# Kernel tuning notes

Measured on AMD Instinct MI355X. Metric: run time of the kernel, lower is better.

The kernel has to match this reference:

```python
import jax, jax.numpy as jnp
import numpy as np

D_MODEL = 2048
N_HEADS = 16
D_HEAD = D_MODEL // N_HEADS


def setup_inputs() -> dict:
    key = jax.random.key(0)
    ks = jax.random.split(key, 9)
    s = 1.0 / np.sqrt(D_MODEL)
    x = jax.random.normal(ks[0], (2, 2048, D_MODEL), dtype=jnp.float32)
    wq = jax.random.uniform(ks[1], (D_MODEL, D_MODEL), jnp.float32, -s, s)
    wk = jax.random.uniform(ks[2], (D_MODEL, D_MODEL), jnp.float32, -s, s)
    wv = jax.random.uniform(ks[3], (D_MODEL, D_MODEL), jnp.float32, -s, s)
    wo = jax.random.uniform(ks[4], (D_MODEL, D_MODEL), jnp.float32, -s, s)
    bq = jax.random.uniform(ks[5], (D_MODEL,), jnp.float32, -s, s)
    bk = jax.random.uniform(ks[6], (D_MODEL,), jnp.float32, -s, s)
    bv = jax.random.uniform(ks[7], (D_MODEL,), jnp.float32, -s, s)
    bo = jax.random.uniform(ks[8], (D_MODEL,), jnp.float32, -s, s)
    return {"x": x, "wq": wq, "bq": bq, "wk": wk, "bk": bk,
            "wv": wv, "bv": bv, "wo": wo, "bo": bo}


def reference(x, wq, bq, wk, bk, wv, bv, wo, bo):
    b, s, _ = x.shape
    # torch Linear: y = x @ W.T + b
    q = (jnp.einsum('bsd,ed->bse', x, wq) + bq).reshape(b, s, N_HEADS, D_HEAD)
    k = (jnp.einsum('bsd,ed->bse', x, wk) + bk).reshape(b, s, N_HEADS, D_HEAD)
    v = (jnp.einsum('bsd,ed->bse', x, wv) + bv).reshape(b, s, N_HEADS, D_HEAD)
    scale = 1.0 / np.sqrt(D_HEAD).astype(np.float32)
    # [b, h, s, s] attention scores (naive full materialization, as in source)
    attn = jnp.einsum('bqhd,bkhd->bhqk', q, k) * scale
    attn = jax.nn.softmax(attn, axis=-1)
    out = jnp.einsum('bhqk,bkhd->bqhd', attn, v).reshape(b, s, D_MODEL)
    return jnp.einsum('bsd,ed->bse', out, wo) + bo
```

## Files before the change

### kernel.cpp

```cpp
#include <hip/hip_runtime.h>

#define D_MODEL 2048
#define SEQ     2048
#define NB      2
#define NH      16
#define DH      128
#define MROWS   (NB*SEQ)
#define GK      2048
#define NT      (GK/64)

typedef __bf16 bf16x8 __attribute__((ext_vector_type(8)));
typedef float  f32x4  __attribute__((ext_vector_type(4)));
typedef unsigned short ushort8 __attribute__((ext_vector_type(8)));
typedef unsigned int   u32x4   __attribute__((ext_vector_type(4)));

__device__ __forceinline__ unsigned short f2bf(float f) {
  unsigned int u = __float_as_uint(f);
  u += 0x7FFFu + ((u >> 16) & 1u);
  return (unsigned short)(u >> 16);
}

__device__ __forceinline__ unsigned int cvtpk_bf16(float lo, float hi) {
  unsigned int r;
  asm("v_cvt_pk_bf16_f32 %0, %1, %2" : "=v"(r) : "v"(lo), "v"(hi));
  return r;
}

__device__ __forceinline__ void gload16(void* lds, const void* g) {
  __builtin_amdgcn_global_load_lds(
      (__attribute__((address_space(1))) void*)(g),
      (__attribute__((address_space(3))) void*)(lds), 16, 0, 0);
}

__global__ __launch_bounds__(256) void cast_all(
    const float* __restrict__ x,
    const float* __restrict__ w0, const float* __restrict__ w1,
    const float* __restrict__ w2, const float* __restrict__ w3,
    unsigned short* __restrict__ xb, unsigned short* __restrict__ wb) {
  int gb = blockIdx.x;
  const float* src;
  unsigned short* dst;
  int i;
  if (gb < 4096) {
    src = x; dst = xb; i = gb * 256 + threadIdx.x;
  } else {
    int g2 = gb - 4096;
    int which = g2 >> 11;
    src = (which == 0) ? w0 : (which == 1) ? w1 : (which == 2) ? w2 : w3;
    dst = wb + (size_t)which * 4194304;
    i = (g2 & 2047) * 256 + threadIdx.x;
  }
  const float4* p = (const float4*)src;
  float4 a = p[2*i], b = p[2*i+1];
  ushort8 o;
  o[0]=f2bf(a.x); o[1]=f2bf(a.y); o[2]=f2bf(a.z); o[3]=f2bf(a.w);
  o[4]=f2bf(b.x); o[5]=f2bf(b.y); o[6]=f2bf(b.z); o[7]=f2bf(b.w);
  ((ushort8*)dst)[i] = o;
}

__global__ __launch_bounds__(512, 2) void gemm192(
    const unsigned short* __restrict__ A,
    const unsigned short* __restrict__ B,
    const float* __restrict__ b0, const float* __restrict__ b1,
    const float* __restrict__ b2,
    unsigned short* __restrict__ qo, unsigned short* __restrict__ ko,
    unsigned short* __restrict__ vo)
{
  __shared__ char lds[2*57344];

  const int tid  = threadIdx.x;
  const int lane = tid & 63, wid = tid >> 6;
  const int la   = lane & 15, hi = lane >> 4;
  const int wm   = wid >> 2,  wn = wid & 3;

  const int xcd = (int)blockIdx.x & 7, ii = (int)blockIdx.x >> 3;
  const int bm  = ii >> 2;
  const int bn  = xcd * 4 + (ii & 3);

  const unsigned short* Ab = A + (size_t)(bm*256) * GK;
  const unsigned short* Bb = B + (size_t)(bn*192) * GK;

  f32x4 acc[8][3];
  #pragma unroll
  for (int m = 0; m < 8; m++)
    #pragma unroll
    for (int n = 0; n < 3; n++) acc[m][n] = f32x4{0.f,0.f,0.f,0.f};

#define STG_A1J(base_, kt, J) do {                                            \
    int idx = (J)*512 + tid;                                                  \
    int row = idx >> 3;                                                       \
    int c   = (idx & 7) << 4;                                                 \
    gload16((base_) + idx*16,                                                 \
            Ab + (size_t)row*GK + (kt)*64 + ((c ^ ((row&7)<<4)) >> 1));       \
  } while (0)

#define STG_BJ(base_, kt, J0, J1) do {                                        \
    _Pragma("unroll")                                                         \
    for (int j = (J0); j < (J1); j++) {                                       \
      int idx = j*512 + tid;                                                  \
      int row = idx >> 3;                                                     \
      int c   = (idx & 7) << 4;                                               \
      gload16((base_) + 32768 + idx*16,                                       \
              Bb + (size_t)row*GK + (kt)*64 + ((c ^ ((row&7)<<4)) >> 1));     \
    }                                                                         \
  } while (0)

  STG_BJ(lds, 0, 0, 3);
  STG_A1J(lds, 0, 0); STG_A1J(lds, 0, 2);
  STG_A1J(lds, 0, 1); STG_A1J(lds, 0, 3);
  asm volatile("s_waitcnt vmcnt(2)" ::: "memory");
  __builtin_amdgcn_s_barrier();

  const int xr = (la & 7) << 4;

  #pragma unroll 1
  for (int t = 0; t < NT; ++t) {
    const char* sa  = lds + (t&1)*57344;
    const char* sbp = sa + 32768;
    char* nb = lds + ((t+1)&1)*57344;
    const bool pf = (t + 1 < NT);

    bf16x8 bfr[3], aq[4];

    #pragma unroll
    for (int n = 0; n < 3; n++)
      bfr[n] = *(const bf16x8*)(sbp + (((wn*48 + n*16 + la)*128 + hi*16) ^ xr));
    #pragma unroll
    for (int m = 0; m < 4; m++)
      aq[m] = *(const bf16x8*)(sa + (((wm*128 + m*16 + la)*128 + hi*16) ^ xr));
    if (pf) STG_BJ(nb, t+1, 0, 3);
    asm volatile("s_waitcnt lgkmcnt(0)" ::: "memory");
    __builtin_amdgcn_sched_barrier(0);
    __builtin_amdgcn_s_setprio(1);
    #pragma unroll
    for (int m = 0; m < 4; m++)
      #pragma unroll
      for (int n = 0; n < 3; n++)
        acc[m][n] = __builtin_amdgcn_mfma_f32_16x16x32_bf16(aq[m], bfr[n], acc[m][n], 0, 0, 0);
    __builtin_amdgcn_s_setprio(0);
    if (pf) asm volatile("s_waitcnt vmcnt(3)" ::: "memory");
    else    asm volatile("s_waitcnt vmcnt(0)" ::: "memory");
    __builtin_amdgcn_s_barrier();

    #pragma unroll
    for (int m = 0; m < 4; m++)
      aq[m] = *(const bf16x8*)(sa + (((wm*128 + (m+4)*16 + la)*128 + hi*16) ^ xr));
    if (pf) { STG_A1J(nb, t+1, 0); STG_A1J(nb, t+1, 2); }
    asm volatile("s_waitcnt lgkmcnt(0)" ::: "memory");
    __builtin_amdgcn_sched_barrier(0);
    __builtin_amdgcn_s_setprio(1);
    #pragma unroll
    for (int m = 0; m < 4; m++)
      #pragma unroll
      for (int n = 0; n < 3; n++)
        acc[m+4][n] = __builtin_amdgcn_mfma_f32_16x16x32_bf16(aq[m], bfr[n], acc[m+4][n], 0, 0, 0);
    __builtin_amdgcn_s_setprio(0);
    __builtin_amdgcn_s_barrier();

    #pragma unroll
    for (int n = 0; n < 3; n++)
      bfr[n] = *(const bf16x8*)(sbp + (((wn*48 + n*16 + la)*128 + 64 + hi*16) ^ xr));
    #pragma unroll
    for (int m = 0; m < 4; m++)
      aq[m] = *(const bf16x8*)(sa + (((wm*128 + m*16 + la)*128 + 64 + hi*16) ^ xr));
    if (pf) { STG_A1J(nb, t+1, 1); STG_A1J(nb, t+1, 3); }
    asm volatile("s_waitcnt lgkmcnt(0)" ::: "memory");
    __builtin_amdgcn_sched_barrier(0);
    __builtin_amdgcn_s_setprio(1);
    #pragma unroll
    for (int m = 0; m < 4; m++)
      #pragma unroll
      for (int n = 0; n < 3; n++)
        acc[m][n] = __builtin_amdgcn_mfma_f32_16x16x32_bf16(aq[m], bfr[n], acc[m][n], 0, 0, 0);
    __builtin_amdgcn_s_setprio(0);
    __builtin_amdgcn_s_barrier();

    #pragma unroll
    for (int m = 0; m < 4; m++)
      aq[m] = *(const bf16x8*)(sa + (((wm*128 + (m+4)*16 + la)*128 + 64 + hi*16) ^ xr));
    asm volatile("s_waitcnt lgkmcnt(0)" ::: "memory");
    __builtin_amdgcn_sched_barrier(0);
    __builtin_amdgcn_s_setprio(1);
    #pragma unroll
    for (int m = 0; m < 4; m++)
      #pragma unroll
      for (int n = 0; n < 3; n++)
        acc[m+4][n] = __builtin_amdgcn_mfma_f32_16x16x32_bf16(aq[m], bfr[n], acc[m+4][n], 0, 0, 0);
    __builtin_amdgcn_s_setprio(0);
    if (pf) asm volatile("s_waitcnt vmcnt(2)" ::: "memory");
    else    asm volatile("s_waitcnt vmcnt(0)" ::: "memory");
    __builtin_amdgcn_s_barrier();
  }
#undef STG_A1J
#undef STG_BJ

  const int row0 = bm*256 + wm*128;
  const int col0 = bn*192 + wn*48;
  #pragma unroll
  for (int n = 0; n < 3; n++) {
    int col = col0 + n*16 + la;
    int mat = col >> 11;
    int c   = col & 2047;
    int h   = c >> 7, d = c & 127;
    const float* bp = (mat == 0) ? b0 : (mat == 1) ? b1 : b2;
    float bv = bp[c];
    #pragma unroll
    for (int m = 0; m < 8; m++)
      #pragma unroll
      for (int r = 0; r < 4; r++) {
        int row = row0 + m*16 + hi*4 + r;
        int bb  = row >> 11, s = row & (SEQ-1);
        unsigned short val = f2bf(acc[m][n][r] + bv);
        if (mat == 0) {
          qo[((size_t)(bb*NH + h)*SEQ + s)*DH + d] = val;
        } else if (mat == 1) {
          size_t base = ((size_t)(bb*NH + h)*SEQ + (size_t)(s >> 6)*64)*DH;
          int boff = (((s & 63) << 8) + (d << 1)) ^ ((s & 7) << 4);
          ko[base + (boff >> 1)] = val;
        } else {
          size_t base = ((size_t)(bb*NH + h)*SEQ + (size_t)(s >> 6)*64)*DH;
          int boff = ((d << 7) + ((s & 63) << 1)) ^ ((d & 7) << 4);
          vo[base + (boff >> 1)] = val;
        }
      }
  }
}

__global__ __launch_bounds__(512, 2) void gemm256(
    const unsigned short* __restrict__ A,
    const unsigned short* __restrict__ B,
    const float* __restrict__ b0,
    float* __restrict__ fo,
    int nbnx)
{
  __shared__ char lds[3*49152];

  const int tid  = threadIdx.x;
  const int lane = tid & 63, wid = tid >> 6;
  const int la   = lane & 15, hi = lane >> 4;
  const int wm   = wid >> 2,  wn = wid & 3;

  const int xcd = (int)blockIdx.x & 7, ii = (int)blockIdx.x >> 3;
  const int bm  = ii / nbnx;
  const int bn  = xcd * nbnx + ii % nbnx;

  const unsigned short* Ab = A + (size_t)(bm*128) * GK;
  const unsigned short* Bb = B + (size_t)(bn*256) * GK;

  f32x4 acc[4][4];
  #pragma unroll
  for (int m = 0; m < 4; m++)
    #pragma unroll
    for (int n = 0; n < 4; n++) acc[m][n] = f32x4{0.f,0.f,0.f,0.f};

#define STAGE_A(slot, kt) do {                                                \
    int sb_ = (slot) * 49152;                                                 \
    _Pragma("unroll")                                                         \
    for (int j = 0; j < 2; j++) {                                             \
      int idx = j*512 + tid;                                                  \
      int row = idx >> 3;                                                     \
      int c   = (idx & 7) << 4;                                               \
      gload16(lds + sb_ + idx*16,                                             \
              Ab + (size_t)row*GK + (kt)*64 + ((c ^ ((row&7)<<4)) >> 1));     \
    }                                                                         \
  } while (0)

#define STAGE_B(slot, kt) do {                                                \
    int sb_ = (slot) * 49152;                                                 \
    _Pragma("unroll")                                                         \
    for (int j = 0; j < 4; j++) {                                             \
      int idx = j*512 + tid;                                                  \
      int row = idx >> 3;                                                     \
      int c   = (idx & 7) << 4;                                               \
      gload16(lds + sb_ + 16384 + idx*16,                                     \
              Bb + (size_t)row*GK + (kt)*64 + ((c ^ ((row&7)<<4)) >> 1));     \
    }                                                                         \
  } while (0)

  STAGE_A(0, 0); STAGE_B(0, 0);
  STAGE_A(1, 1); STAGE_B(1, 1);

  int cs = 0, ps = 2;
  const int xr = (la & 7) << 4;

  #pragma unroll 1
  for (int t = 0; t < NT; ++t) {
    if (t + 1 < NT) asm volatile("s_waitcnt vmcnt(6)" ::: "memory");
    else            asm volatile("s_waitcnt vmcnt(0)" ::: "memory");
    __builtin_amdgcn_s_barrier();

    const char* sa  = lds + cs*49152;
    const char* sbp = sa + 16384;

    bf16x8 bfr[4][2], aA[2][2];
    #pragma unroll
    for (int n = 0; n < 4; n++)
      #pragma unroll
      for (int ks = 0; ks < 2; ks++)
        bfr[n][ks] = *(const bf16x8*)(sbp + (((wn*64 + n*16 + la)*128 + ks*64 + hi*16) ^ xr));
    #pragma unroll
    for (int m = 0; m < 2; m++)
      #pragma unroll
      for (int ks = 0; ks < 2; ks++)
        aA[m][ks] = *(const bf16x8*)(sa + (((wm*64 + m*16 + la)*128 + ks*64 + hi*16) ^ xr));

    if (t + 2 < NT) STAGE_A(ps, t + 2);

    asm volatile("s_waitcnt lgkmcnt(0)" ::: "memory");
    __builtin_amdgcn_sched_barrier(0);
    __builtin_amdgcn_s_setprio(1);
    #pragma unroll
    for (int m = 0; m < 2; m++)
      #pragma unroll
      for (int n = 0; n < 4; n++)
        #pragma unroll
        for (int ks = 0; ks < 2; ks++)
          acc[m][n] = __builtin_amdgcn_mfma_f32_16x16x32_bf16(aA[m][ks], bfr[n][ks], acc[m][n], 0, 0, 0);
    __builtin_amdgcn_s_setprio(0);
    __builtin_amdgcn_s_barrier();

    bf16x8 aB[2][2];
    #pragma unroll
    for (int m = 0; m < 2; m++)
      #pragma unroll
      for (int ks = 0; ks < 2; ks++)
        aB[m][ks] = *(const bf16x8*)(sa + (((wm*64 + (m+2)*16 + la)*128 + ks*64 + hi*16) ^ xr));

    if (t + 2 < NT) STAGE_B(ps, t + 2);

    asm volatile("s_waitcnt lgkmcnt(0)" ::: "memory");
    __builtin_amdgcn_sched_barrier(0);
    __builtin_amdgcn_s_setprio(1);
    #pragma unroll
    for (int m = 0; m < 2; m++)
      #pragma unroll
      for (int n = 0; n < 4; n++)
        #pragma unroll
        for (int ks = 0; ks < 2; ks++)
          acc[m+2][n] = __builtin_amdgcn_mfma_f32_16x16x32_bf16(aB[m][ks], bfr[n][ks], acc[m+2][n], 0, 0, 0);
    __builtin_amdgcn_s_setprio(0);

    cs = cs + 1; if (cs == 3) cs = 0;
    ps = ps + 1; if (ps == 3) ps = 0;
  }
#undef STAGE_A
#undef STAGE_B

  const int row0 = bm*128 + wm*64;
  const int col0 = bn*256 + wn*64;
  #pragma unroll
  for (int n = 0; n < 4; n++) {
    int col = col0 + n*16 + la;
    float bv = b0[col];
    #pragma unroll
    for (int m = 0; m < 4; m++)
      #pragma unroll
      for (int r = 0; r < 4; r++) {
        int row = row0 + m*16 + hi*4 + r;
        fo[(size_t)row*D_MODEL + col] = acc[m][n][r] + bv;
      }
  }
}

__global__ __launch_bounds__(256, 2) void attn_fwd(
    const unsigned short* __restrict__ Q,
    const unsigned short* __restrict__ Kg,
    const unsigned short* __restrict__ VTg,
    unsigned short* __restrict__ O)
{
  __shared__ unsigned short Ks [2][64*128];
  __shared__ unsigned short VTs[2][128*64];

  const int tid  = threadIdx.x;
  const int lane = tid & 63, wid = tid >> 6;
  const int la   = lane & 15, hi = lane >> 4;
  const int swz  = ((int)(blockIdx.x & 7) << 6) + ((int)blockIdx.x >> 3);
  const int bh   = swz >> 4;
  const int q0   = (swz & 15) << 7;
  const int b    = bh >> 4, h = bh & 15;

  const unsigned short* Qh = Q   + (size_t)bh * SEQ * DH;
  const unsigned short* Kh = Kg  + (size_t)bh * SEQ * DH;
  const unsigned short* Vh = VTg + (size_t)bh * SEQ * DH;

  const int qrow = q0 + wid * 32;

  bf16x8 qf[2][4];
  #pragma unroll
  for (int qi = 0; qi < 2; qi++)
    #pragma unroll
    for (int ks = 0; ks < 4; ks++)
      qf[qi][ks] = *(const bf16x8*)(Qh + (size_t)(qrow + qi*16 + la)*DH + ks*32 + hi*8);

  f32x4 o[2][8];
  float mrun[2], lrun[2];
  #pragma unroll
  for (int qi = 0; qi < 2; qi++) {
    #pragma unroll
    for (int df = 0; df < 8; df++) o[qi][df] = f32x4{0.f,0.f,0.f,0.f};
    mrun[qi] = -1e30f; lrun[qi] = 0.f;
  }

  #pragma unroll
  for (int i = 0; i < 4; i++) {
    int off = i*4096 + tid*16;
    gload16((char*)Ks[0]  + off, (const char*)Kh + off);
    gload16((char*)VTs[0] + off, (const char*)Vh + off);
  }
  __syncthreads();

  const float sc2 = 0.1275424483f;

  #pragma unroll 1
  for (int t = 0; t < SEQ/64; ++t) {
    const int cur = t & 1;

    if (t + 1 < SEQ/64) {
      const char* kt = (const char*)(Kh + (size_t)(t+1)*(64*DH));
      const char* vt = (const char*)(Vh + (size_t)(t+1)*(64*DH));
      #pragma unroll
      for (int i = 0; i < 4; i++) {
        int off = i*4096 + tid*16;
        gload16((char*)Ks[cur^1]  + off, kt + off);
        gload16((char*)VTs[cur^1] + off, vt + off);
      }
    }

    f32x4 S[4][2];
    #pragma unroll
    for (int mf = 0; mf < 4; mf++)
      #pragma unroll
      for (int qi = 0; qi < 2; qi++) S[mf][qi] = f32x4{0.f,0.f,0.f,0.f};
    #pragma unroll
    for (int ks = 0; ks < 4; ks++) {
      bf16x8 kf[4];
      #pragma unroll
      for (int mf = 0; mf < 4; mf++) {
        int boff = (((mf*16 + la) << 8) + (ks << 6) + (hi << 4)) ^ ((la & 7) << 4);
        kf[mf] = *(const bf16x8*)((const char*)Ks[cur] + boff);
      }
      #pragma unroll
      for (int mf = 0; mf < 4; mf++)
        #pragma unroll
        for (int qi = 0; qi < 2; qi++)
          S[mf][qi] = __builtin_amdgcn_mfma_f32_16x16x32_bf16(kf[mf], qf[qi][ks], S[mf][qi], 0, 0, 0);
    }

    unsigned int pf[2][2][4];
    #pragma unroll
    for (int qi = 0; qi < 2; qi++) {
      float pm = S[0][qi][0];
      #pragma unroll
      for (int mf = 0; mf < 4; mf++)
        #pragma unroll
        for (int r = 0; r < 4; r++) pm = fmaxf(pm, S[mf][qi][r]);
      pm = fmaxf(pm, __shfl_xor(pm, 16));
      pm = fmaxf(pm, __shfl_xor(pm, 32));
      pm *= sc2;

      float mn;
      if (__all(pm <= mrun[qi] + 8.0f)) {
        mn = mrun[qi];
      } else {
        mn = fmaxf(mrun[qi], pm);
        float alpha = __builtin_amdgcn_exp2f(mrun[qi] - mn);
        mrun[qi] = mn;
        lrun[qi] *= alpha;
        #pragma unroll
        for (int r = 0; r < 4; r++) {
          float ar = __shfl(alpha, (lane & 48) | ((hi << 2) | r), 64);
          #pragma unroll
          for (int df = 0; df < 8; df++) o[qi][df][r] *= ar;
        }
      }

      float p[4][4]; float rs = 0.f;
      #pragma unroll
      for (int mf = 0; mf < 4; mf++)
        #pragma unroll
        for (int r = 0; r < 4; r++) {
          float e = __builtin_amdgcn_exp2f(fmaf(S[mf][qi][r], sc2, -mn));
          p[mf][r] = e; rs += e;
        }
      rs += __shfl_xor(rs, 16);
      rs += __shfl_xor(rs, 32);
      lrun[qi] += rs;

      unsigned int c[4][2];
      #pragma unroll
      for (int mf = 0; mf < 4; mf++) {
        c[mf][0] = cvtpk_bf16(p[mf][0], p[mf][1]);
        c[mf][1] = cvtpk_bf16(p[mf][2], p[mf][3]);
      }
      #pragma unroll
      for (int ks2 = 0; ks2 < 2; ks2++) {
        #pragma unroll
        for (int w = 0; w < 4; w++) {
          int src = la + 16*(2*(hi & 1) + (w >> 1));
          unsigned int t0 = __shfl(c[2*ks2    ][w & 1], src, 64);
          unsigned int t1 = __shfl(c[2*ks2 + 1][w & 1], src, 64);
          pf[qi][ks2][w] = (hi >> 1) ? t1 : t0;
        }
      }
    }

    #pragma unroll
    for (int ks2 = 0; ks2 < 2; ks2++) {
      #pragma unroll
      for (int df = 0; df < 8; df++) {
        int vrow = df*16 + la;
        int boff = ((vrow << 7) + (ks2 << 6) + (hi << 4)) ^ ((la & 7) << 4);
        bf16x8 vf = *(const bf16x8*)((const char*)VTs[cur] + boff);
        #pragma unroll
        for (int qi = 0; qi < 2; qi++) {
          u32x4 pw = {pf[qi][ks2][0], pf[qi][ks2][1], pf[qi][ks2][2], pf[qi][ks2][3]};
          o[qi][df] = __builtin_amdgcn_mfma_f32_16x16x32_bf16(
              __builtin_bit_cast(bf16x8, pw), vf, o[qi][df], 0, 0, 0);
        }
      }
    }
    __syncthreads();
  }

  unsigned short* Ob = O + (size_t)b * SEQ * D_MODEL + h * DH;
  #pragma unroll
  for (int qi = 0; qi < 2; qi++) {
    float linv[4];
    #pragma unroll
    for (int r = 0; r < 4; r++)
      linv[r] = 1.0f / __shfl(lrun[qi], (lane & 48) | ((hi << 2) | r), 64);
    #pragma unroll
    for (int df = 0; df < 8; df++)
      #pragma unroll
      for (int r = 0; r < 4; r++) {
        int srow = qrow + qi*16 + hi*4 + r;
        Ob[(size_t)srow * D_MODEL + df*16 + la] = f2bf(o[qi][df][r] * linv[r]);
      }
  }
}

extern "C" void kernel_launch(void* const* d_in, const int* in_sizes, int n_in,
                              void* d_out, int out_size, void* d_ws, size_t ws_size,
                              hipStream_t stream) {
  const float* x  = (const float*)d_in[0];
  const float* wq = (const float*)d_in[1];
  const float* bq = (const float*)d_in[2];
  const float* wk = (const float*)d_in[3];
  const float* bk = (const float*)d_in[4];
  const float* wv = (const float*)d_in[5];
  const float* bv = (const float*)d_in[6];
  const float* wo = (const float*)d_in[7];
  const float* bo = (const float*)d_in[8];
  float* out = (float*)d_out;

  const size_t X = (size_t)MROWS * D_MODEL;
  const size_t W = (size_t)D_MODEL * D_MODEL;

  unsigned short* ws  = (unsigned short*)d_ws;
  unsigned short* xb  = ws;
  unsigned short* wqb = xb  + X;
  unsigned short* wkb = wqb + W;
  unsigned short* wvb = wkb + W;
  unsigned short* wob = wvb + W;
  unsigned short* qb  = wob + W;
  unsigned short* kb  = qb  + X;
  unsigned short* vtg = kb  + X;
  unsigned short* ab  = vtg + X;

  cast_all<<<dim3(12288), 256, 0, stream>>>(x, wq, wk, wv, wo, xb, wqb);

  gemm192<<<dim3(512), 512, 0, stream>>>(xb, wqb, bq, bk, bv, qb, kb, vtg);

  attn_fwd<<<dim3(512), 256, 0, stream>>>(qb, kb, vtg, ab);

  gemm256<<<dim3(256), 512, 0, stream>>>(ab, wob, bo, out, 1);
}
```

Measured before the change: 269.7 us.

## Restructure output-projection GEMM to 256x128 tiles with double-buffered split prefetch

The output projection GEMM changes from 128x256 block tiles with a 3-slot LDS ring to 256x128 tiles with two LDS buffers. Each k-tile is split into four MFMA phases, and the next tile's B and A loads are interleaved between them, with waits placed to overlap global loads and compute. The intent is a lower LDS footprint and a finer-grained load/compute schedule, at the cost of more barriers per k-tile and a different block-to-XCD mapping.

```diff
diff --git a/kernel.cpp b/kernel.cpp
--- a/kernel.cpp
+++ b/kernel.cpp
@@ -226,14 +226,13 @@
   }
 }
 
-__global__ __launch_bounds__(512, 2) void gemm256(
+__global__ __launch_bounds__(512, 2) void gemmop(
     const unsigned short* __restrict__ A,
     const unsigned short* __restrict__ B,
     const float* __restrict__ b0,
-    float* __restrict__ fo,
-    int nbnx)
+    float* __restrict__ fo)
 {
-  __shared__ char lds[3*49152];
+  __shared__ char lds[2*49152];
 
   const int tid  = threadIdx.x;
   const int lane = tid & 63, wid = tid >> 6;
@@ -241,119 +240,134 @@
   const int wm   = wid >> 2,  wn = wid & 3;
 
   const int xcd = (int)blockIdx.x & 7, ii = (int)blockIdx.x >> 3;
-  const int bm  = ii / nbnx;
-  const int bn  = xcd * nbnx + ii % nbnx;
-
-  const unsigned short* Ab = A + (size_t)(bm*128) * GK;
-  const unsigned short* Bb = B + (size_t)(bn*256) * GK;
-
-  f32x4 acc[4][4];
-  #pragma unroll
-  for (int m = 0; m < 4; m++)
-    #pragma unroll
-    for (int n = 0; n < 4; n++) acc[m][n] = f32x4{0.f,0.f,0.f,0.f};
-
-#define STAGE_A(slot, kt) do {                                                \
-    int sb_ = (slot) * 49152;                                                 \
+  const int bm  = ii >> 1;
+  const int bn  = xcd * 2 + (ii & 1);
+
+  const unsigned short* Ab = A + (size_t)(bm*256) * GK;
+  const unsigned short* Bb = B + (size_t)(bn*128) * GK;
+
+  f32x4 acc[8][2];
+  #pragma unroll
+  for (int m = 0; m < 8; m++)
+    #pragma unroll
+    for (int n = 0; n < 2; n++) acc[m][n] = f32x4{0.f,0.f,0.f,0.f};
+
+#define OP_A1J(base_, kt, J) do {                                             \
+    int idx = (J)*512 + tid;                                                  \
+    int row = idx >> 3;                                                       \
+    int c   = (idx & 7) << 4;                                                 \
+    gload16((base_) + idx*16,                                                 \
+            Ab + (size_t)row*GK + (kt)*64 + ((c ^ ((row&7)<<4)) >> 1));       \
+  } while (0)
+
+#define OP_BJ(base_, kt) do {                                                 \
     _Pragma("unroll")                                                         \
     for (int j = 0; j < 2; j++) {                                             \
       int idx = j*512 + tid;                                                  \
       int row = idx >> 3;                                                     \
       int c   = (idx & 7) << 4;                                               \
-      gload16(lds + sb_ + idx*16,                                             \
-              Ab + (size_t)row*GK + (kt)*64 + ((c ^ ((row&7)<<4)) >> 1));     \
-    }                                                                         \
-  } while (0)
-
-#define STAGE_B(slot, kt) do {                                                \
-    int sb_ = (slot) * 49152;                                                 \
-    _Pragma("unroll")                                                         \
-    for (int j = 0; j < 4; j++) {                                             \
-      int idx = j*512 + tid;                                                  \
-      int row = idx >> 3;                                                     \
-      int c   = (idx & 7) << 4;                                               \
-      gload16(lds + sb_ + 16384 + idx*16,                                     \
+      gload16((base_) + 32768 + idx*16,                                       \
               Bb + (size_t)row*GK + (kt)*64 + ((c ^ ((row&7)<<4)) >> 1));     \
     }                                                                         \
   } while (0)
 
-  STAGE_A(0, 0); STAGE_B(0, 0);
-  STAGE_A(1, 1); STAGE_B(1, 1);
-
-  int cs = 0, ps = 2;
+  OP_BJ(lds, 0);
+  OP_A1J(lds, 0, 0); OP_A1J(lds, 0, 2);
+  OP_A1J(lds, 0, 1); OP_A1J(lds, 0, 3);
+  asm volatile("s_waitcnt vmcnt(2)" ::: "memory");
+  __builtin_amdgcn_s_barrier();
+
   const int xr = (la & 7) << 4;
 
   #pragma unroll 1
   for (int t = 0; t < NT; ++t) {
-    if (t + 1 < NT) asm volatile("s_waitcnt vmcnt(6)" ::: "memory");
-    else            asm volatile("s_waitcnt vmcnt(0)" ::: "memory");
-    __builtin_amdgcn_s_barrier();
-
-    const char* sa  = lds + cs*49152;
-    const char* sbp = sa + 16384;
-
-    bf16x8 bfr[4][2], aA[2][2];
-    #pragma unroll
-    for (int n = 0; n < 4; n++)
-      #pragma unroll
-      for (int ks = 0; ks < 2; ks++)
-        bfr[n][ks] = *(const bf16x8*)(sbp + (((wn*64 + n*16 + la)*128 + ks*64 + hi*16) ^ xr));
-    #pragma unroll
-    for (int m = 0; m < 2; m++)
-      #pragma unroll
-      for (int ks = 0; ks < 2; ks++)
-        aA[m][ks] = *(const bf16x8*)(sa + (((wm*64 + m*16 + la)*128 + ks*64 + hi*16) ^ xr));
-
-    if (t + 2 < NT) STAGE_A(ps, t + 2);
-
-    asm volatile("s_waitcnt lgkmcnt(0)" ::: "memory");
-    __builtin_amdgcn_sched_barrier(0);
-    __builtin_amdgcn_s_setprio(1);
-    #pragma unroll
-    for (int m = 0; m < 2; m++)
-      #pragma unroll
-      for (int n = 0; n < 4; n++)
-        #pragma unroll
-        for (int ks = 0; ks < 2; ks++)
-          acc[m][n] = __builtin_amdgcn_mfma_f32_16x16x32_bf16(aA[m][ks], bfr[n][ks], acc[m][n], 0, 0, 0);
-    __builtin_amdgcn_s_setprio(0);
-    __builtin_amdgcn_s_barrier();
-
-    bf16x8 aB[2][2];
-    #pragma unroll
-    for (int m = 0; m < 2; m++)
-      #pragma unroll
-      for (int ks = 0; ks < 2; ks++)
-        aB[m][ks] = *(const bf16x8*)(sa + (((wm*64 + (m+2)*16 + la)*128 + ks*64 + hi*16) ^ xr));
-
-    if (t + 2 < NT) STAGE_B(ps, t + 2);
-
-    asm volatile("s_waitcnt lgkmcnt(0)" ::: "memory");
-    __builtin_amdgcn_sched_barrier(0);
-    __builtin_amdgcn_s_setprio(1);
-    #pragma unroll
-    for (int m = 0; m < 2; m++)
-      #pragma unroll
-      for (int n = 0; n < 4; n++)
-        #pragma unroll
-        for (int ks = 0; ks < 2; ks++)
-          acc[m+2][n] = __builtin_amdgcn_mfma_f32_16x16x32_bf16(aB[m][ks], bfr[n][ks], acc[m+2][n], 0, 0, 0);
-    __builtin_amdgcn_s_setprio(0);
-
-    cs = cs + 1; if (cs == 3) cs = 0;
-    ps = ps + 1; if (ps == 3) ps = 0;
-  }
-#undef STAGE_A
-#undef STAGE_B
-
-  const int row0 = bm*128 + wm*64;
-  const int col0 = bn*256 + wn*64;
-  #pragma unroll
-  for (int n = 0; n < 4; n++) {
+    const char* sa  = lds + (t&1)*49152;
+    const char* sbp = sa + 32768;
+    char* nb = lds + ((t+1)&1)*49152;
+    const bool pf = (t + 1 < NT);
+
+    bf16x8 bfr[2], aq[4];
+
+    #pragma unroll
+    for (int n = 0; n < 2; n++)
+      bfr[n] = *(const bf16x8*)(sbp + (((wn*32 + n*16 + la)*128 + hi*16) ^ xr));
+    #pragma unroll
+    for (int m = 0; m < 4; m++)
+      aq[m] = *(const bf16x8*)(sa + (((wm*128 + m*16 + la)*128 + hi*16) ^ xr));
+    if (pf) OP_BJ(nb, t+1);
+    asm volatile("s_waitcnt lgkmcnt(0)" ::: "memory");
+    __builtin_amdgcn_sched_barrier(0);
+    __builtin_amdgcn_s_setprio(1);
+    #pragma unroll
+    for (int m = 0; m < 4; m++)
+      #pragma unroll
+      for (int n = 0; n < 2; n++)
+        acc[m][n] = __builtin_amdgcn_mfma_f32_16x16x32_bf16(aq[m], bfr[n], acc[m][n], 0, 0, 0);
+    __builtin_amdgcn_s_setprio(0);
+    if (pf) asm volatile("s_waitcnt vmcnt(2)" ::: "memory");
+    else    asm volatile("s_waitcnt vmcnt(0)" ::: "memory");
+    __builtin_amdgcn_s_barrier();
+
+    #pragma unroll
+    for (int m = 0; m < 4; m++)
+      aq[m] = *(const bf16x8*)(sa + (((wm*128 + (m+4)*16 + la)*128 + hi*16) ^ xr));
+    if (pf) { OP_A1J(nb, t+1, 0); OP_A1J(nb, t+1, 2); }
+    asm volatile("s_waitcnt lgkmcnt(0)" ::: "memory");
+    __builtin_amdgcn_sched_barrier(0);
+    __builtin_amdgcn_s_setprio(1);
+    #pragma unroll
+    for (int m = 0; m < 4; m++)
+      #pragma unroll
+      for (int n = 0; n < 2; n++)
+        acc[m+4][n] = __builtin_amdgcn_mfma_f32_16x16x32_bf16(aq[m], bfr[n], acc[m+4][n], 0, 0, 0);
+    __builtin_amdgcn_s_setprio(0);
+    __builtin_amdgcn_s_barrier();
+
+    #pragma unroll
+    for (int n = 0; n < 2; n++)
+      bfr[n] = *(const bf16x8*)(sbp + (((wn*32 + n*16 + la)*128 + 64 + hi*16) ^ xr));
+    #pragma unroll
+    for (int m = 0; m < 4; m++)
+      aq[m] = *(const bf16x8*)(sa + (((wm*128 + m*16 + la)*128 + 64 + hi*16) ^ xr));
+    if (pf) { OP_A1J(nb, t+1, 1); OP_A1J(nb, t+1, 3); }
+    asm volatile("s_waitcnt lgkmcnt(0)" ::: "memory");
+    __builtin_amdgcn_sched_barrier(0);
+    __builtin_amdgcn_s_setprio(1);
+    #pragma unroll
+    for (int m = 0; m < 4; m++)
+      #pragma unroll
+      for (int n = 0; n < 2; n++)
+        acc[m][n] = __builtin_amdgcn_mfma_f32_16x16x32_bf16(aq[m], bfr[n], acc[m][n], 0, 0, 0);
+    __builtin_amdgcn_s_setprio(0);
+    __builtin_amdgcn_s_barrier();
+
+    #pragma unroll
+    for (int m = 0; m < 4; m++)
+      aq[m] = *(const bf16x8*)(sa + (((wm*128 + (m+4)*16 + la)*128 + 64 + hi*16) ^ xr));
+    asm volatile("s_waitcnt lgkmcnt(0)" ::: "memory");
+    __builtin_amdgcn_sched_barrier(0);
+    __builtin_amdgcn_s_setprio(1);
+    #pragma unroll
+    for (int m = 0; m < 4; m++)
+      #pragma unroll
+      for (int n = 0; n < 2; n++)
+        acc[m+4][n] = __builtin_amdgcn_mfma_f32_16x16x32_bf16(aq[m], bfr[n], acc[m+4][n], 0, 0, 0);
+    __builtin_amdgcn_s_setprio(0);
+    if (pf) asm volatile("s_waitcnt vmcnt(2)" ::: "memory");
+    else    asm volatile("s_waitcnt vmcnt(0)" ::: "memory");
+    __builtin_amdgcn_s_barrier();
+  }
+#undef OP_A1J
+#undef OP_BJ
+
+  const int row0 = bm*256 + wm*128;
+  const int col0 = bn*128 + wn*32;
+  #pragma unroll
+  for (int n = 0; n < 2; n++) {
     int col = col0 + n*16 + la;
     float bv = b0[col];
     #pragma unroll
-    for (int m = 0; m < 4; m++)
+    for (int m = 0; m < 8; m++)
       #pragma unroll
       for (int r = 0; r < 4; r++) {
         int row = row0 + m*16 + hi*4 + r;
@@ -573,5 +587,5 @@
 
   attn_fwd<<<dim3(512), 256, 0, stream>>>(qb, kb, vtg, ab);
 
-  gemm256<<<dim3(256), 512, 0, stream>>>(ab, wob, bo, out, 1);
-}
+  gemmop<<<dim3(256), 512, 0, stream>>>(ab, wob, bo, out);
+}
```

Measured after the change: 272.5 us. About the same (+1.0%).

## Single-buffer V tile to fit three attention workgroups per CU

Applied to the files above, without the earlier changes.

The V^T shared tile drops from double to single buffering, which cuts LDS from 64KB to 48KB per block, and launch bounds rise to 3 blocks per SM. Each iteration now issues the current V tile load alongside the next K prefetch and waits on it with explicit vmcnt and barrier just before the PV MFMAs. More resident waves are meant to hide latency, but V load latency is now exposed within the iteration and tighter register limits may cause spills.

```diff
diff --git a/kernel.cpp b/kernel.cpp
--- a/kernel.cpp
+++ b/kernel.cpp
@@ -362,14 +362,14 @@
   }
 }
 
-__global__ __launch_bounds__(256, 2) void attn_fwd(
+__global__ __launch_bounds__(256, 3) void attn_fwd(
     const unsigned short* __restrict__ Q,
     const unsigned short* __restrict__ Kg,
     const unsigned short* __restrict__ VTg,
     unsigned short* __restrict__ O)
 {
   __shared__ unsigned short Ks [2][64*128];
-  __shared__ unsigned short VTs[2][128*64];
+  __shared__ unsigned short VTs[128*64];
 
   const int tid  = threadIdx.x;
   const int lane = tid & 63, wid = tid >> 6;
@@ -404,25 +404,32 @@
   #pragma unroll
   for (int i = 0; i < 4; i++) {
     int off = i*4096 + tid*16;
-    gload16((char*)Ks[0]  + off, (const char*)Kh + off);
-    gload16((char*)VTs[0] + off, (const char*)Vh + off);
-  }
-  __syncthreads();
+    gload16((char*)Ks[0] + off, (const char*)Kh + off);
+  }
+  asm volatile("s_waitcnt vmcnt(0)" ::: "memory");
+  __builtin_amdgcn_s_barrier();
 
   const float sc2 = 0.1275424483f;
 
   #pragma unroll 1
   for (int t = 0; t < SEQ/64; ++t) {
     const int cur = t & 1;
-
-    if (t + 1 < SEQ/64) {
-      const char* kt = (const char*)(Kh + (size_t)(t+1)*(64*DH));
-      const char* vt = (const char*)(Vh + (size_t)(t+1)*(64*DH));
+    const bool pf = (t + 1 < SEQ/64);
+
+    {
+      const char* vt = (const char*)(Vh + (size_t)t*(64*DH));
       #pragma unroll
       for (int i = 0; i < 4; i++) {
         int off = i*4096 + tid*16;
-        gload16((char*)Ks[cur^1]  + off, kt + off);
-        gload16((char*)VTs[cur^1] + off, vt + off);
+        gload16((char*)VTs + off, vt + off);
+      }
+      if (pf) {
+        const char* kt = (const char*)(Kh + (size_t)(t+1)*(64*DH));
+        #pragma unroll
+        for (int i = 0; i < 4; i++) {
+          int off = i*4096 + tid*16;
+          gload16((char*)Ks[cur^1] + off, kt + off);
+        }
       }
     }
 
@@ -446,7 +453,7 @@
           S[mf][qi] = __builtin_amdgcn_mfma_f32_16x16x32_bf16(kf[mf], qf[qi][ks], S[mf][qi], 0, 0, 0);
     }
 
-    unsigned int pf[2][2][4];
+    unsigned int pf2[2][2][4];
     #pragma unroll
     for (int qi = 0; qi < 2; qi++) {
       float pm = S[0][qi][0];
@@ -499,10 +506,14 @@
           int src = la + 16*(2*(hi & 1) + (w >> 1));
           unsigned int t0 = __shfl(c[2*ks2    ][w & 1], src, 64);
           unsigned int t1 = __shfl(c[2*ks2 + 1][w & 1], src, 64);
-          pf[qi][ks2][w] = (hi >> 1) ? t1 : t0;
+          pf2[qi][ks2][w] = (hi >> 1) ? t1 : t0;
         }
       }
     }
+
+    if (pf) asm volatile("s_waitcnt vmcnt(4)" ::: "memory");
+    else    asm volatile("s_waitcnt vmcnt(0)" ::: "memory");
+    __builtin_amdgcn_s_barrier();
 
     #pragma unroll
     for (int ks2 = 0; ks2 < 2; ks2++) {
@@ -510,16 +521,18 @@
       for (int df = 0; df < 8; df++) {
         int vrow = df*16 + la;
         int boff = ((vrow << 7) + (ks2 << 6) + (hi << 4)) ^ ((la & 7) << 4);
-        bf16x8 vf = *(const bf16x8*)((const char*)VTs[cur] + boff);
+        bf16x8 vf = *(const bf16x8*)((const char*)VTs + boff);
         #pragma unroll
         for (int qi = 0; qi < 2; qi++) {
-          u32x4 pw = {pf[qi][ks2][0], pf[qi][ks2][1], pf[qi][ks2][2], pf[qi][ks2][3]};
+          u32x4 pw = {pf2[qi][ks2][0], pf2[qi][ks2][1], pf2[qi][ks2][2], pf2[qi][ks2][3]};
           o[qi][df] = __builtin_amdgcn_mfma_f32_16x16x32_bf16(
               __builtin_bit_cast(bf16x8, pw), vf, o[qi][df], 0, 0, 0);
         }
       }
     }
-    __syncthreads();
+
+    asm volatile("s_waitcnt vmcnt(0)" ::: "memory");
+    __builtin_amdgcn_s_barrier();
   }
 
   unsigned short* Ob = O + (size_t)b * SEQ * D_MODEL + h * DH;
```

New measurement: 338.6 us. 25.6% more time.
